# Performance work log

Measured on AMD Instinct MI355X. Metric: run time of the kernel, lower is better.

## Reference

```python
import jax, jax.numpy as jnp
import numpy as np

B, S, D = 2, 1024, 1024
H, HD = 16, 64
E_R = 31          # routed experts (n_experts - n_shared)
K_ACT = 3         # activated routed experts (n_activated - n_shared)
INTER = 1024      # expert inter dim = int(D*4*0.25)
EPS = 1e-5
BASE = 10000.0


def setup_inputs() -> dict:
    key = jax.random.key(0)
    ks = jax.random.split(key, 24)
    s = 0.02
    theta = (BASE ** (-jnp.arange(HD // 2, dtype=jnp.float32) * 2.0 / HD))
    inp = {
        'x': jax.random.normal(ks[0], (B, S, D), jnp.float32),
        'positions': jnp.arange(S, dtype=jnp.int32),
        'theta': theta,
        'gamma1': jnp.ones((D,), jnp.float32),
        'gamma2': jnp.ones((D,), jnp.float32),
        'q_w': jax.random.normal(ks[1], (D, H * HD), jnp.float32) * s,
        'q_b': jnp.zeros((H * HD,), jnp.float32),
        'k_w': jax.random.normal(ks[2], (D, H * HD), jnp.float32) * s,
        'k_b': jnp.zeros((H * HD,), jnp.float32),
        'v_w': jax.random.normal(ks[3], (D, H * HD), jnp.float32) * s,
        'v_b': jnp.zeros((H * HD,), jnp.float32),
        'o_w': jax.random.normal(ks[4], (H * HD, D), jnp.float32) * s,
        'o_b': jnp.zeros((D,), jnp.float32),
        'router_w': jax.random.normal(ks[5], (D, E_R), jnp.float32) * s,
        'router_b': jnp.zeros((E_R,), jnp.float32),
        'sh_w1': jax.random.normal(ks[6], (D, INTER), jnp.float32) * s,
        'sh_b1': jnp.zeros((INTER,), jnp.float32),
        'sh_w2': jax.random.normal(ks[7], (INTER, D), jnp.float32) * s,
        'sh_b2': jnp.zeros((D,), jnp.float32),
        're_w1': jax.random.normal(ks[8], (E_R, D, INTER), jnp.float32) * s,
        're_b1': jnp.zeros((E_R, INTER), jnp.float32),
        're_w2': jax.random.normal(ks[9], (E_R, INTER, D), jnp.float32) * s,
        're_b2': jnp.zeros((E_R, D), jnp.float32),
    }
    return inp


def _rmsnorm(x, gamma):
    rms = jnp.sqrt(jnp.mean(x * x, axis=-1, keepdims=True) + EPS)
    return x / rms * gamma


def _rope(x, theta):
    # x: [B,H,S,HD]; split even/odd, rotate, concat halves (matches source)
    seq = x.shape[2]
    angles = jnp.arange(seq, dtype=theta.dtype)[:, None] * theta  # [S, HD/2]
    cos = jnp.cos(angles)[None, None]
    sin = jnp.sin(angles)[None, None]
    x1, x2 = x[..., 0::2], x[..., 1::2]
    return jnp.concatenate([x1 * cos - x2 * sin, x1 * sin + x2 * cos], axis=-1)


def _forward(x, theta, gamma1, gamma2, q_w, q_b, k_w, k_b, v_w, v_b, o_w, o_b,
             router_w, router_b, sh_w1, sh_b1, sh_w2, sh_b2,
             re_w1, re_b1, re_w2, re_b2):
    b, s, d = x.shape
    xn = _rmsnorm(x, gamma1)
    # --- MHA ---
    q = (xn @ q_w + q_b).reshape(b, s, H, HD).transpose(0, 2, 1, 3)
    k = (xn @ k_w + k_b).reshape(b, s, H, HD).transpose(0, 2, 1, 3)
    v = (xn @ v_w + v_b).reshape(b, s, H, HD).transpose(0, 2, 1, 3)
    q = _rope(q, theta)
    k = _rope(k, theta)
    scale = 1.0 / np.sqrt(HD)
    scores = jnp.einsum('bhqd,bhkd->bhqk', q, k) * scale
    causal = jnp.tril(jnp.ones((s, s), dtype=bool))
    scores = jnp.where(causal, scores, -jnp.inf)
    attn = jax.nn.softmax(scores, axis=-1)
    ctx = jnp.einsum('bhqk,bhkd->bhqd', attn, v)
    ctx = ctx.transpose(0, 2, 1, 3).reshape(b, s, H * HD)
    attn_out = ctx @ o_w + o_b + xn
    # --- MoE ---
    an = _rmsnorm(attn_out, gamma2)
    shared = jax.nn.gelu(an @ sh_w1 + sh_b1, approximate=False) @ sh_w2 + sh_b2
    logits = an @ router_w + router_b                      # [B,S,E]
    aff = jax.nn.softmax(logits, axis=-1)
    topv, topi = jax.lax.top_k(aff, K_ACT)                 # [B,S,K]
    gates = jnp.sum(jax.nn.one_hot(topi, E_R, dtype=aff.dtype) * topv[..., None], axis=-2)  # [B,S,E]
    h = jax.nn.gelu(jnp.einsum('bsd,edh->besh', an, re_w1) + re_b1[None, :, None, :],
                    approximate=False)                     # [B,E,S,INTER]
    routed = jnp.einsum('bse,besh,ehd->bsd', gates, h, re_w2) \
           + jnp.einsum('bse,ed->bsd', gates, re_b2)
    return shared + routed + an + attn_out


def reference(x, positions, theta, gamma1, gamma2, q_w, q_b, k_w, k_b, v_w, v_b,
              o_w, o_b, router_w, router_b, sh_w1, sh_b1, sh_w2, sh_b2,
              re_w1, re_b1, re_w2, re_b2):
    del positions  # unused by the original forward (RoPE builds its own arange)
    return _forward(x, theta, gamma1, gamma2, q_w, q_b, k_w, k_b, v_w, v_b,
                    o_w, o_b, router_w, router_b, sh_w1, sh_b1, sh_w2, sh_b2,
                    re_w1, re_b1, re_w2, re_b2)
```

## Files before the change

### kernel.cpp

```cpp
#include <hip/hip_runtime.h>
#include <math.h>

typedef unsigned short u16;
typedef short s8v __attribute__((ext_vector_type(8)));
typedef u16 u4v __attribute__((ext_vector_type(4)));
typedef float f4v __attribute__((ext_vector_type(4)));

#define MFMA16(a,b,c) __builtin_amdgcn_mfma_f32_16x16x32_bf16((a),(b),(c),0,0,0)
#define GLDS16(g, l) __builtin_amdgcn_global_load_lds( \
    (const __attribute__((address_space(1))) unsigned int*)(g), \
    (__attribute__((address_space(3))) unsigned int*)(l), 16, 0, 0)

#define N_TOK 2048
#define SEQ   1024

__device__ __forceinline__ u16 f2b(float f){
  union { float f; unsigned u; } v; v.f = f;
  return (u16)((v.u + 0x7FFFu + ((v.u >> 16) & 1u)) >> 16);
}
__device__ __forceinline__ float b2f(u16 b){
  union { unsigned u; float f; } v; v.u = ((unsigned)b) << 16; return v.f;
}
__device__ __forceinline__ float gelu_f(float x){
  return 0.5f*x*(1.0f + erff(x*0.70710678118654752f));
}

__global__ __launch_bounds__(256) void rmsnorm_k(const float* __restrict__ x,
    const float* __restrict__ gamma, float* __restrict__ outf, u16* __restrict__ outb)
{
  const int t = blockIdx.x, tid = threadIdx.x;
  const float* xr = x + (size_t)t * 1024;
  float4 xv = *(const float4*)(xr + tid*4);
  float ss = xv.x*xv.x + xv.y*xv.y + xv.z*xv.z + xv.w*xv.w;
  #pragma unroll
  for (int off = 32; off; off >>= 1) ss += __shfl_down(ss, off);
  __shared__ float red[4];
  if ((tid & 63) == 0) red[tid >> 6] = ss;
  __syncthreads();
  float inv = rsqrtf((red[0]+red[1]+red[2]+red[3]) * (1.0f/1024.0f) + 1e-5f);
  float4 gv = *(const float4*)(gamma + tid*4);
  float4 o;
  o.x = xv.x*inv*gv.x; o.y = xv.y*inv*gv.y; o.z = xv.z*inv*gv.z; o.w = xv.w*inv*gv.w;
  *(float4*)(outf + (size_t)t*1024 + tid*4) = o;
  u4v ob = { f2b(o.x), f2b(o.y), f2b(o.z), f2b(o.w) };
  *(u4v*)(outb + (size_t)t*1024 + tid*4) = ob;
}

__global__ __launch_bounds__(256) void ropetab_k(const float* __restrict__ theta, float* __restrict__ tab)
{
  int i = blockIdx.x*256 + threadIdx.x;
  int s = i >> 5, j = i & 31;
  float sn, cs;
  sincosf((float)s * theta[j], &sn, &cs);
  tab[(size_t)s*64 + 2*j]     = cs;
  tab[(size_t)s*64 + 2*j + 1] = sn;
}

__device__ __forceinline__ void transT_body(const float* __restrict__ W, u16* __restrict__ Wt)
{
  __shared__ __align__(16) u16 T[64][68];
  const int tid = threadIdx.x;
  const int k0 = blockIdx.x*64, n0 = blockIdx.y*64;
  #pragma unroll
  for (int j = 0; j < 4; j++) {
    int q = j*256 + tid; int r = q >> 4, c4 = q & 15;
    float4 v = *(const float4*)(W + (size_t)(k0 + r)*1024 + n0 + c4*4);
    T[c4*4+0][r] = f2b(v.x); T[c4*4+1][r] = f2b(v.y);
    T[c4*4+2][r] = f2b(v.z); T[c4*4+3][r] = f2b(v.w);
  }
  __syncthreads();
  #pragma unroll
  for (int j = 0; j < 4; j++) {
    int q = j*256 + tid; int n = q >> 4, c4 = q & 15;
    u4v o = *(const u4v*)&T[n][c4*4];
    *(u4v*)(Wt + (size_t)(n0 + n)*1024 + k0 + c4*4) = o;
  }
}

__global__ __launch_bounds__(256) void transT6_k(
    const float* s0, const float* s1, const float* s2,
    const float* s3, const float* s4, const float* s5,
    u16* d0, u16* d1, u16* d2, u16* d3, u16* d4, u16* d5)
{
  const float* S; u16* D;
  switch (blockIdx.z) {
    case 0: S=s0; D=d0; break; case 1: S=s1; D=d1; break;
    case 2: S=s2; D=d2; break; case 3: S=s3; D=d3; break;
    case 4: S=s4; D=d4; break; default: S=s5; D=d5; break;
  }
  transT_body(S, D);
}

__global__ __launch_bounds__(256) void transv_k(const u16* __restrict__ vb, u16* __restrict__ vt)
{
  __shared__ __align__(16) u16 T[64][72];
  const int tid = threadIdx.x;
  const int s0 = blockIdx.x*64, bh = blockIdx.y, b = bh>>4, h = bh&15;
  #pragma unroll
  for (int j = 0; j < 16; j++) {
    int q = j*256 + tid; int r = q >> 6, c = q & 63;
    T[c][r] = vb[(size_t)(b*SEQ + s0 + r)*1024 + h*64 + c];
  }
  __syncthreads();
  #pragma unroll
  for (int i = 0; i < 2; i++) {
    int q = tid*2 + i; int rr = q >> 3, c8 = q & 7;
    *(s8v*)(vt + (size_t)(bh*64 + rr)*1024 + s0 + c8*8) = *(const s8v*)&T[rr][c8*8];
  }
}

template<int MODE, int BM, int BN>
__global__ __launch_bounds__(256) void mmk(
    const u16* __restrict__ A,
    const u16* __restrict__ Wt0, const u16* __restrict__ Wt1, const u16* __restrict__ Wt2,
    const float* __restrict__ bias0, const float* __restrict__ bias1, const float* __restrict__ bias2,
    float* __restrict__ outf, u16* __restrict__ outb0, u16* __restrict__ outb1, u16* __restrict__ outb2,
    const float* __restrict__ add1, const float* __restrict__ add2,
    const int* __restrict__ gidx, const float* __restrict__ gatel,
    const int* __restrict__ counts, const int* __restrict__ offs,
    const int* __restrict__ wl, const int* __restrict__ ntl,
    const float* __restrict__ theta, const float* __restrict__ wf)
{
  constexpr bool EW = (MODE == 5 || MODE == 6);
  constexpr int MF = BM/32, NF = BN/32;
  constexpr int CA = BM/32, CB = BN/32;
  constexpr int BST = EW ? 72 : 64;
  __shared__ __align__(16) u16 As[BM*64];
  __shared__ __align__(16) u16 Bs[BN*BST];
  __shared__ int toks[(MODE==5) ? BM : 1];
  __shared__ float gts[(MODE==6) ? BM : 1];

  const int tid = threadIdx.x;
  const int wave = tid >> 6, lane = tid & 63, quad = lane >> 4, l15 = lane & 15;
  int row0 = blockIdx.y * BM;
  int col0 = blockIdx.x * BN;
  const u16* Wt = Wt0;
  const float* bias = bias0;
  const u16* Ab = A;
  const float* Wf = wf;
  int wsel = 0, e = 0, cnt = 0, off_e = 0;

  if (MODE == 7) {
    wsel = blockIdx.x >> 3;
    col0 = (blockIdx.x & 7) * BN;
    Wt   = (wsel == 0) ? Wt0 : ((wsel == 1) ? Wt1 : Wt2);
    bias = (wsel == 0) ? bias0 : ((wsel == 1) ? bias1 : bias2);
  }
  if (EW) {
    if ((int)blockIdx.y >= ntl[0]) return;
    const int w = wl[blockIdx.y];
    e = w >> 8;
    row0 = (w & 255) * BM;
    cnt = counts[e];
    Wf = wf + (size_t)e * 1024 * 1024;
    bias = bias0 + e * 1024;
    off_e = offs[e];
    if (MODE == 6) Ab = A + (size_t)off_e * 1024;
    if (tid < BM) {
      int ok = (row0 + tid) < cnt;
      if (MODE == 5) toks[tid] = ok ? gidx[e * N_TOK + row0 + tid] : 0;
      if (MODE == 6) gts[tid]  = ok ? gatel[e * N_TOK + row0 + tid] : 0.f;
    }
    __syncthreads();
  }

  const int lr8 = lane >> 3;
  const int lk  = (lane & 7) * 8;
  const u16* aptr[CA];
  const u16* bptr[CB];
  #pragma unroll
  for (int c = 0; c < CA; c++) {
    const int ar = wave*(BM/4) + c*8 + lr8;
    long garow;
    if (MODE == 5) {
      garow = toks[ar];
    } else if (MODE == 6) {
      int rr = row0 + ar; if (rr >= cnt) rr = cnt - 1; garow = rr;
    } else {
      garow = row0 + ar;
    }
    aptr[c] = Ab + (size_t)garow * 1024 + lk;
  }
  if (!EW) {
    #pragma unroll
    for (int c = 0; c < CB; c++) {
      const int br = wave*(BN/4) + c*8 + lr8;
      bptr[c] = Wt + (size_t)(col0 + br) * 1024 + lk;
    }
  }

  const int ewnb = tid >> 3;
  const int ewkb = tid & 7;
  const float* ewp = EW ? (Wf + (size_t)(ewkb*8)*1024 + col0 + ewnb*4) : nullptr;

  f4v acc[MF][NF];
  #pragma unroll
  for (int i = 0; i < MF; i++)
    #pragma unroll
    for (int j = 0; j < NF; j++)
      acc[i][j] = (f4v){0.f,0.f,0.f,0.f};

  const int wr = (wave >> 1) * (BM/2), wc = (wave & 1) * (BN/2);

  for (int k0 = 0; k0 < 1024; k0 += 64) {
    float4 f[EW ? 8 : 1];
    if (EW) {
      const float* wp = ewp + (size_t)k0 * 1024;
      #pragma unroll
      for (int kk = 0; kk < 8; kk++)
        f[kk] = *(const float4*)(wp + (size_t)kk * 1024);
    }
    __syncthreads();
    #pragma unroll
    for (int c = 0; c < CA; c++) GLDS16(aptr[c] + k0, As + (wave*(BM/4) + c*8)*64);
    if (EW) {
      #pragma unroll
      for (int j = 0; j < 4; j++) {
        s8v h;
        #pragma unroll
        for (int kk = 0; kk < 8; kk++) {
          float fv = (j == 0) ? f[kk].x : (j == 1) ? f[kk].y : (j == 2) ? f[kk].z : f[kk].w;
          h[kk] = (short)f2b(fv);
        }
        *(s8v*)&Bs[(ewnb*4 + j)*BST + ewkb*8] = h;
      }
    } else {
      #pragma unroll
      for (int c = 0; c < CB; c++) GLDS16(bptr[c] + k0, Bs + (wave*(BN/4) + c*8)*64);
    }
    __syncthreads();
    s8v af[2][MF], bfr[2][NF];
    #pragma unroll
    for (int ks = 0; ks < 2; ks++) {
      #pragma unroll
      for (int mt = 0; mt < MF; mt++) af[ks][mt]  = *(const s8v*)&As[(wr + mt*16 + l15)*64 + ks*32 + quad*8];
      #pragma unroll
      for (int nt = 0; nt < NF; nt++) bfr[ks][nt] = *(const s8v*)&Bs[(wc + nt*16 + l15)*BST + ks*32 + quad*8];
    }
    #pragma unroll
    for (int ks = 0; ks < 2; ks++)
      #pragma unroll
      for (int mt = 0; mt < MF; mt++)
        #pragma unroll
        for (int nt = 0; nt < NF; nt++)
          acc[mt][nt] = MFMA16(af[ks][mt], bfr[ks][nt], acc[mt][nt]);
  }

  #pragma unroll
  for (int mt = 0; mt < MF; mt++) {
    #pragma unroll
    for (int reg = 0; reg < 4; reg++) {
      const int lr = wr + mt*16 + quad*4 + reg;
      const size_t gr = row0 + lr;
      #pragma unroll
      for (int nt = 0; nt < NF; nt++) {
        const int n = wc + nt*16 + l15 + col0;
        float v = acc[mt][nt][reg] + bias[n];
        if (MODE == 7) {
          if (wsel == 2) {
            outb2[gr*1024 + n] = f2b(v);
          } else {
            float pv = __shfl_xor(v, 1);
            const int hd = n & 63;
            const int j = hd >> 1;
            const int s = (int)(gr & (SEQ - 1));
            float2 t = *(const float2*)&theta[(size_t)s*64 + 2*j];
            float cs = t.x, sn = t.y;
            float res; int col;
            if (hd & 1) { res = pv*sn + v*cs; col = (n & ~63) | (32 + j); }
            else        { res = v*cs - pv*sn; col = (n & ~63) | j; }
            u16 bv = f2b(res);
            if (wsel == 0) outb0[gr*1024 + col] = bv;
            else           outb1[gr*1024 + col] = bv;
          }
        } else if (MODE == 3) {
          outf[gr*1024 + n] = v + add1[gr*1024 + n];
        } else if (MODE == 2) {
          outb0[gr*1024 + n] = f2b(gelu_f(v));
        } else if (MODE == 4) {
          outf[gr*1024 + n] = v + add1[gr*1024 + n] + add2[gr*1024 + n];
        } else if (MODE == 5) {
          if (row0 + lr < cnt)
            outb0[(size_t)(off_e + row0 + lr)*1024 + n] = f2b(gelu_f(v));
        } else if (MODE == 6) {
          if (row0 + lr < cnt)
            outf[(size_t)(off_e + row0 + lr)*1024 + n] = gts[lr] * v;
        }
      }
    }
  }
}

__global__ __launch_bounds__(256) void attn_k(const u16* __restrict__ qg,
    const u16* __restrict__ kg, const u16* __restrict__ vtg, u16* __restrict__ ctx)
{
  const int qt = (blockIdx.y < 16) ? blockIdx.x : (15 - blockIdx.x);
  const int bh = blockIdx.y, b = bh >> 4, h = bh & 15;
  const int tid = threadIdx.x, wave = tid >> 6, lane = tid & 63;
  const int quad = lane >> 4, l15 = lane & 15;
  __shared__ __align__(16) u16 Ks[64][72];
  __shared__ __align__(16) u16 Vt[64][72];
  __shared__ __align__(16) u16 Ps[4][16][72];

  s8v aq0, aq1;
  {
    const size_t qrow = (size_t)(b*SEQ + qt*64 + wave*16 + l15);
    aq0 = *(const s8v*)(qg + qrow*1024 + h*64 + quad*8);
    aq1 = *(const s8v*)(qg + qrow*1024 + h*64 + 32 + quad*8);
  }
  f4v oac[4];
  #pragma unroll
  for (int i = 0; i < 4; i++) oac[i] = (f4v){0.f,0.f,0.f,0.f};
  float mi[4] = {-INFINITY,-INFINITY,-INFINITY,-INFINITY};
  float li[4] = {0.f,0.f,0.f,0.f};

  for (int kt = 0; kt <= qt; kt++) {
    __syncthreads();
    #pragma unroll
    for (int ii = 0; ii < 2; ii++) {
      int c = tid*2 + ii, r = c >> 3, c8 = c & 7;
      *(s8v*)&Ks[r][c8*8] = *(const s8v*)(kg + (size_t)(b*SEQ + kt*64 + r)*1024 + h*64 + c8*8);
      *(s8v*)&Vt[r][c8*8] = *(const s8v*)(vtg + (size_t)(bh*64 + r)*1024 + kt*64 + c8*8);
    }
    __syncthreads();

    f4v s[4];
    #pragma unroll
    for (int nt = 0; nt < 4; nt++) {
      f4v z = (f4v){0.f,0.f,0.f,0.f};
      s8v bk0 = *(const s8v*)&Ks[nt*16 + l15][quad*8];
      s8v bk1 = *(const s8v*)&Ks[nt*16 + l15][32 + quad*8];
      z = MFMA16(aq0, bk0, z);
      z = MFMA16(aq1, bk1, z);
      s[nt] = z;
    }
    float sc[4][4];
    const int rowl = wave*16 + quad*4;
    #pragma unroll
    for (int nt = 0; nt < 4; nt++) {
      #pragma unroll
      for (int r = 0; r < 4; r++) {
        float v = s[nt][r] * 0.125f;
        if (kt == qt && (nt*16 + l15) > (rowl + r)) v = -INFINITY;
        sc[nt][r] = v;
      }
    }
    float alpha[4];
    #pragma unroll
    for (int r = 0; r < 4; r++) {
      float v0 = fmaxf(fmaxf(sc[0][r], sc[1][r]), fmaxf(sc[2][r], sc[3][r]));
      v0 = fmaxf(v0, __shfl_xor(v0, 1));
      v0 = fmaxf(v0, __shfl_xor(v0, 2));
      v0 = fmaxf(v0, __shfl_xor(v0, 4));
      v0 = fmaxf(v0, __shfl_xor(v0, 8));
      float mnew = fmaxf(mi[r], v0);
      alpha[r] = __expf(mi[r] - mnew);
      mi[r] = mnew;
    }
    float psum[4] = {0.f,0.f,0.f,0.f};
    #pragma unroll
    for (int nt = 0; nt < 4; nt++) {
      #pragma unroll
      for (int r = 0; r < 4; r++) {
        float p = __expf(sc[nt][r] - mi[r]);
        psum[r] += p;
        Ps[wave][quad*4 + r][nt*16 + l15] = f2b(p);
      }
    }
    #pragma unroll
    for (int r = 0; r < 4; r++) {
      float ps = psum[r];
      ps += __shfl_xor(ps, 1);
      ps += __shfl_xor(ps, 2);
      ps += __shfl_xor(ps, 4);
      ps += __shfl_xor(ps, 8);
      li[r] = li[r]*alpha[r] + ps;
    }
    #pragma unroll
    for (int ht = 0; ht < 4; ht++) {
      f4v o = oac[ht];
      o[0] *= alpha[0]; o[1] *= alpha[1]; o[2] *= alpha[2]; o[3] *= alpha[3];
      oac[ht] = o;
    }
    asm volatile("s_waitcnt lgkmcnt(0)" ::: "memory");
    s8v pf0 = *(const s8v*)&Ps[wave][l15][quad*8];
    s8v pf1 = *(const s8v*)&Ps[wave][l15][32 + quad*8];
    #pragma unroll
    for (int ht = 0; ht < 4; ht++) {
      s8v vf0 = *(const s8v*)&Vt[ht*16 + l15][quad*8];
      s8v vf1 = *(const s8v*)&Vt[ht*16 + l15][32 + quad*8];
      oac[ht] = MFMA16(pf0, vf0, oac[ht]);
      oac[ht] = MFMA16(pf1, vf1, oac[ht]);
    }
  }
  float inv[4];
  #pragma unroll
  for (int r = 0; r < 4; r++) inv[r] = 1.f / li[r];
  #pragma unroll
  for (int ht = 0; ht < 4; ht++) {
    #pragma unroll
    for (int r = 0; r < 4; r++) {
      size_t row = (size_t)(b*SEQ + qt*64 + wave*16 + quad*4 + r);
      ctx[row*1024 + h*64 + ht*16 + l15] = f2b(oac[ht][r] * inv[r]);
    }
  }
}

__global__ __launch_bounds__(256) void router_k(const float* __restrict__ an,
    const float* __restrict__ rw, const float* __restrict__ rb,
    int* __restrict__ counts, int* __restrict__ tok_list, float* __restrict__ gate_list,
    int* __restrict__ tok_e, int* __restrict__ tok_s)
{
  const int t = blockIdx.x, tid = threadIdx.x;
  const int e = tid & 31, ch = tid >> 5;
  float part = 0.f;
  if (e < 31) {
    const float* ar = an + (size_t)t*1024 + ch*128;
    const float* wp = rw + (size_t)(ch*128)*31 + e;
    #pragma unroll 8
    for (int d = 0; d < 128; d++) part += ar[d] * wp[d*31];
  }
  __shared__ float red[8][32];
  __shared__ float lgs[32];
  red[ch][e] = part;
  __syncthreads();
  if (tid < 31) {
    float s = 0.f;
    #pragma unroll
    for (int c = 0; c < 8; c++) s += red[c][tid];
    lgs[tid] = s + rb[tid];
  }
  __syncthreads();
  if (tid == 0) {
    float m = -1e30f;
    for (int i = 0; i < 31; i++) m = fmaxf(m, lgs[i]);
    float den = 0.f;
    for (int i = 0; i < 31; i++) den += __expf(lgs[i] - m);
    float invd = 1.f/den;
    unsigned used = 0;
    for (int kk = 0; kk < 3; kk++) {
      int best = 0; float bv = -3e30f;
      for (int i = 0; i < 31; i++) if (!((used>>i)&1u) && lgs[i] > bv) { bv = lgs[i]; best = i; }
      used |= (1u << best);
      float gate = __expf(lgs[best] - m) * invd;
      int slot = atomicAdd(&counts[best], 1);
      tok_list[best*N_TOK + slot] = t;
      gate_list[best*N_TOK + slot] = gate;
      tok_e[t*3 + kk] = best;
      tok_s[t*3 + kk] = slot;
    }
  }
}

__global__ void scan_k(const int* __restrict__ counts, int* __restrict__ offs,
                       int* __restrict__ wl, int* __restrict__ ntl){
  if (threadIdx.x == 0) {
    int s = 0, nt = 0;
    for (int i = 0; i < 31; i++){
      offs[i] = s; s += counts[i];
      int t = (counts[i] + 127) >> 7;
      for (int r = 0; r < t; r++) wl[nt++] = (i << 8) | r;
    }
    ntl[0] = nt;
  }
}

__global__ __launch_bounds__(256) void reduce_k(const float* __restrict__ mo,
    const int* __restrict__ tok_e, const int* __restrict__ tok_s,
    const int* __restrict__ offs, float* __restrict__ out)
{
  const int t = blockIdx.x, tid = threadIdx.x;
  float4 acc = *(const float4*)(out + (size_t)t*1024 + tid*4);
  #pragma unroll
  for (int j = 0; j < 3; j++) {
    int e = tok_e[t*3 + j], s = tok_s[t*3 + j];
    const float* row = mo + (size_t)(offs[e] + s) * 1024;
    float4 v = *(const float4*)(row + tid*4);
    acc.x += v.x; acc.y += v.y; acc.z += v.z; acc.w += v.w;
  }
  *(float4*)(out + (size_t)t*1024 + tid*4) = acc;
}

extern "C" void kernel_launch(void* const* d_in, const int* in_sizes, int n_in,
                              void* d_out, int out_size, void* d_ws, size_t ws_size,
                              hipStream_t stream)
{
  const float* x      = (const float*)d_in[0];
  const float* theta  = (const float*)d_in[2];
  const float* gamma1 = (const float*)d_in[3];
  const float* gamma2 = (const float*)d_in[4];
  const float* q_w = (const float*)d_in[5];
  const float* q_b = (const float*)d_in[6];
  const float* k_w = (const float*)d_in[7];
  const float* k_b = (const float*)d_in[8];
  const float* v_w = (const float*)d_in[9];
  const float* v_b = (const float*)d_in[10];
  const float* o_w = (const float*)d_in[11];
  const float* o_b = (const float*)d_in[12];
  const float* router_w = (const float*)d_in[13];
  const float* router_b = (const float*)d_in[14];
  const float* sh_w1 = (const float*)d_in[15];
  const float* sh_b1 = (const float*)d_in[16];
  const float* sh_w2 = (const float*)d_in[17];
  const float* sh_b2 = (const float*)d_in[18];
  const float* re_w1 = (const float*)d_in[19];
  const float* re_b1 = (const float*)d_in[20];
  const float* re_w2 = (const float*)d_in[21];
  const float* re_b2 = (const float*)d_in[22];
  float* out = (float*)d_out;

  char* p = (char*)d_ws;
  auto alloc = [&](size_t bytes) -> void* {
    void* r = (void*)p; p += (bytes + 255) & ~(size_t)255; return r;
  };
  const size_t F32 = (size_t)N_TOK*1024*4;
  const size_t B16 = (size_t)N_TOK*1024*2;
  float* xn       = (float*)alloc(F32);
  float* attn_out = (float*)alloc(F32);
  float* an       = (float*)alloc(F32);
  float* mo       = (float*)alloc((size_t)3*N_TOK*1024*4);
  u16* xnb  = (u16*)alloc(B16);
  u16* anb  = (u16*)alloc(B16);
  u16* vb   = (u16*)alloc(B16);
  u16* qb   = (u16*)alloc(B16);
  u16* kb   = (u16*)alloc(B16);
  u16* vt   = (u16*)alloc(B16);
  u16* ctxb = (u16*)alloc(B16);
  u16* shhb = (u16*)alloc(B16);
  u16* hmoe = (u16*)alloc((size_t)3*N_TOK*1024*2);
  u16* wtq  = (u16*)alloc((size_t)1024*1024*2);
  u16* wtk  = (u16*)alloc((size_t)1024*1024*2);
  u16* wtv  = (u16*)alloc((size_t)1024*1024*2);
  u16* wto  = (u16*)alloc((size_t)1024*1024*2);
  u16* wts1 = (u16*)alloc((size_t)1024*1024*2);
  u16* wts2 = (u16*)alloc((size_t)1024*1024*2);
  float* ropetab = (float*)alloc((size_t)SEQ*64*4);
  int* counts = (int*)alloc(128);
  int* offs   = (int*)alloc(128);
  int* tok_list  = (int*)alloc((size_t)31*N_TOK*4);
  float* gate_list = (float*)alloc((size_t)31*N_TOK*4);
  int* tok_e = (int*)alloc((size_t)N_TOK*3*4);
  int* tok_s = (int*)alloc((size_t)N_TOK*3*4);
  int* wl    = (int*)alloc(512);
  int* ntl   = (int*)alloc(64);

  hipMemsetAsync(counts, 0, 128, stream);

  transT6_k<<<dim3(16,16,6), 256, 0, stream>>>(q_w, k_w, v_w, o_w, sh_w1, sh_w2,
                                               wtq, wtk, wtv, wto, wts1, wts2);
  ropetab_k<<<(SEQ*32)/256, 256, 0, stream>>>(theta, ropetab);

  rmsnorm_k<<<N_TOK, 256, 0, stream>>>(x, gamma1, xn, xnb);

  mmk<7,64,128><<<dim3(24,32), 256, 0, stream>>>(xnb, wtq, wtk, wtv, q_b, k_b, v_b,
      nullptr, qb, kb, vb, nullptr, nullptr, nullptr, nullptr, nullptr, nullptr, nullptr, nullptr,
      ropetab, nullptr);

  transv_k<<<dim3(16,32), 256, 0, stream>>>(vb, vt);
  attn_k<<<dim3(16,32), 256, 0, stream>>>(qb, kb, vt, ctxb);

  mmk<3,64,64><<<dim3(16,32), 256, 0, stream>>>(ctxb, wto, nullptr, nullptr, o_b, nullptr, nullptr,
      attn_out, nullptr, nullptr, nullptr, xn, nullptr, nullptr, nullptr, nullptr, nullptr, nullptr, nullptr,
      nullptr, nullptr);

  rmsnorm_k<<<N_TOK, 256, 0, stream>>>(attn_out, gamma2, an, anb);

  mmk<2,64,64><<<dim3(16,32), 256, 0, stream>>>(anb, wts1, nullptr, nullptr, sh_b1, nullptr, nullptr,
      nullptr, shhb, nullptr, nullptr, nullptr, nullptr, nullptr, nullptr, nullptr, nullptr, nullptr, nullptr,
      nullptr, nullptr);

  router_k<<<N_TOK, 256, 0, stream>>>(an, router_w, router_b, counts, tok_list, gate_list, tok_e, tok_s);
  scan_k<<<1, 32, 0, stream>>>(counts, offs, wl, ntl);

  mmk<4,64,64><<<dim3(16,32), 256, 0, stream>>>(shhb, wts2, nullptr, nullptr, sh_b2, nullptr, nullptr,
      out, nullptr, nullptr, nullptr, an, attn_out, nullptr, nullptr, nullptr, nullptr, nullptr, nullptr,
      nullptr, nullptr);

  mmk<5,128,128><<<dim3(8,79), 256, 0, stream>>>(anb, nullptr, nullptr, nullptr, re_b1, nullptr, nullptr,
      nullptr, hmoe, nullptr, nullptr, nullptr, nullptr, tok_list, nullptr, counts, offs, wl, ntl,
      nullptr, re_w1);

  mmk<6,128,128><<<dim3(8,79), 256, 0, stream>>>(hmoe, nullptr, nullptr, nullptr, re_b2, nullptr, nullptr,
      mo, nullptr, nullptr, nullptr, nullptr, nullptr, tok_list, gate_list, counts, offs, wl, ntl,
      nullptr, re_w2);

  reduce_k<<<N_TOK, 256, 0, stream>>>(mo, tok_e, tok_s, offs, out);
}
```

Baseline: 564.4 us.

## Merge shared-expert and routed-expert GEMMs into combined launches with packed bf16 conversion

The shared-expert FFN GEMMs and the routed-expert grouped GEMMs now run in a single kernel launch per layer (fused_k), with blockIdx.y selecting dense or expert work. This cuts the launch count and lets the shared and routed work fill the GPU together. The shared GEMMs move from 64x64 to 128x128 tiles, and the fp32-to-bf16 weight conversion uses the packed v_cvt_pk_bf16_f32 instruction instead of scalar rounding. In exchange, the larger tiles give the dense part fewer blocks, and blocks with mixed work types may run unevenly.

```diff
diff --git a/kernel.cpp b/kernel.cpp
--- a/kernel.cpp
+++ b/kernel.cpp
@@ -5,6 +5,7 @@
 typedef short s8v __attribute__((ext_vector_type(8)));
 typedef u16 u4v __attribute__((ext_vector_type(4)));
 typedef float f4v __attribute__((ext_vector_type(4)));
+typedef unsigned u32x4 __attribute__((ext_vector_type(4)));
 
 #define MFMA16(a,b,c) __builtin_amdgcn_mfma_f32_16x16x32_bf16((a),(b),(c),0,0,0)
 #define GLDS16(g, l) __builtin_amdgcn_global_load_lds( \
@@ -115,20 +116,13 @@
     const u16* __restrict__ Wt0, const u16* __restrict__ Wt1, const u16* __restrict__ Wt2,
     const float* __restrict__ bias0, const float* __restrict__ bias1, const float* __restrict__ bias2,
     float* __restrict__ outf, u16* __restrict__ outb0, u16* __restrict__ outb1, u16* __restrict__ outb2,
-    const float* __restrict__ add1, const float* __restrict__ add2,
-    const int* __restrict__ gidx, const float* __restrict__ gatel,
-    const int* __restrict__ counts, const int* __restrict__ offs,
-    const int* __restrict__ wl, const int* __restrict__ ntl,
-    const float* __restrict__ theta, const float* __restrict__ wf)
-{
-  constexpr bool EW = (MODE == 5 || MODE == 6);
+    const float* __restrict__ add1,
+    const float* __restrict__ theta)
+{
   constexpr int MF = BM/32, NF = BN/32;
   constexpr int CA = BM/32, CB = BN/32;
-  constexpr int BST = EW ? 72 : 64;
   __shared__ __align__(16) u16 As[BM*64];
-  __shared__ __align__(16) u16 Bs[BN*BST];
-  __shared__ int toks[(MODE==5) ? BM : 1];
-  __shared__ float gts[(MODE==6) ? BM : 1];
+  __shared__ __align__(16) u16 Bs[BN*64];
 
   const int tid = threadIdx.x;
   const int wave = tid >> 6, lane = tid & 63, quad = lane >> 4, l15 = lane & 15;
@@ -136,9 +130,7 @@
   int col0 = blockIdx.x * BN;
   const u16* Wt = Wt0;
   const float* bias = bias0;
-  const u16* Ab = A;
-  const float* Wf = wf;
-  int wsel = 0, e = 0, cnt = 0, off_e = 0;
+  int wsel = 0;
 
   if (MODE == 7) {
     wsel = blockIdx.x >> 3;
@@ -146,23 +138,6 @@
     Wt   = (wsel == 0) ? Wt0 : ((wsel == 1) ? Wt1 : Wt2);
     bias = (wsel == 0) ? bias0 : ((wsel == 1) ? bias1 : bias2);
   }
-  if (EW) {
-    if ((int)blockIdx.y >= ntl[0]) return;
-    const int w = wl[blockIdx.y];
-    e = w >> 8;
-    row0 = (w & 255) * BM;
-    cnt = counts[e];
-    Wf = wf + (size_t)e * 1024 * 1024;
-    bias = bias0 + e * 1024;
-    off_e = offs[e];
-    if (MODE == 6) Ab = A + (size_t)off_e * 1024;
-    if (tid < BM) {
-      int ok = (row0 + tid) < cnt;
-      if (MODE == 5) toks[tid] = ok ? gidx[e * N_TOK + row0 + tid] : 0;
-      if (MODE == 6) gts[tid]  = ok ? gatel[e * N_TOK + row0 + tid] : 0.f;
-    }
-    __syncthreads();
-  }
 
   const int lr8 = lane >> 3;
   const int lk  = (lane & 7) * 8;
@@ -171,27 +146,13 @@
   #pragma unroll
   for (int c = 0; c < CA; c++) {
     const int ar = wave*(BM/4) + c*8 + lr8;
-    long garow;
-    if (MODE == 5) {
-      garow = toks[ar];
-    } else if (MODE == 6) {
-      int rr = row0 + ar; if (rr >= cnt) rr = cnt - 1; garow = rr;
-    } else {
-      garow = row0 + ar;
-    }
-    aptr[c] = Ab + (size_t)garow * 1024 + lk;
-  }
-  if (!EW) {
-    #pragma unroll
-    for (int c = 0; c < CB; c++) {
-      const int br = wave*(BN/4) + c*8 + lr8;
-      bptr[c] = Wt + (size_t)(col0 + br) * 1024 + lk;
-    }
-  }
-
-  const int ewnb = tid >> 3;
-  const int ewkb = tid & 7;
-  const float* ewp = EW ? (Wf + (size_t)(ewkb*8)*1024 + col0 + ewnb*4) : nullptr;
+    aptr[c] = A + (size_t)(row0 + ar) * 1024 + lk;
+  }
+  #pragma unroll
+  for (int c = 0; c < CB; c++) {
+    const int br = wave*(BN/4) + c*8 + lr8;
+    bptr[c] = Wt + (size_t)(col0 + br) * 1024 + lk;
+  }
 
   f4v acc[MF][NF];
   #pragma unroll
@@ -203,31 +164,11 @@
   const int wr = (wave >> 1) * (BM/2), wc = (wave & 1) * (BN/2);
 
   for (int k0 = 0; k0 < 1024; k0 += 64) {
-    float4 f[EW ? 8 : 1];
-    if (EW) {
-      const float* wp = ewp + (size_t)k0 * 1024;
-      #pragma unroll
-      for (int kk = 0; kk < 8; kk++)
-        f[kk] = *(const float4*)(wp + (size_t)kk * 1024);
-    }
     __syncthreads();
     #pragma unroll
     for (int c = 0; c < CA; c++) GLDS16(aptr[c] + k0, As + (wave*(BM/4) + c*8)*64);
-    if (EW) {
-      #pragma unroll
-      for (int j = 0; j < 4; j++) {
-        s8v h;
-        #pragma unroll
-        for (int kk = 0; kk < 8; kk++) {
-          float fv = (j == 0) ? f[kk].x : (j == 1) ? f[kk].y : (j == 2) ? f[kk].z : f[kk].w;
-          h[kk] = (short)f2b(fv);
-        }
-        *(s8v*)&Bs[(ewnb*4 + j)*BST + ewkb*8] = h;
-      }
-    } else {
-      #pragma unroll
-      for (int c = 0; c < CB; c++) GLDS16(bptr[c] + k0, Bs + (wave*(BN/4) + c*8)*64);
-    }
+    #pragma unroll
+    for (int c = 0; c < CB; c++) GLDS16(bptr[c] + k0, Bs + (wave*(BN/4) + c*8)*64);
     __syncthreads();
     s8v af[2][MF], bfr[2][NF];
     #pragma unroll
@@ -235,7 +176,7 @@
       #pragma unroll
       for (int mt = 0; mt < MF; mt++) af[ks][mt]  = *(const s8v*)&As[(wr + mt*16 + l15)*64 + ks*32 + quad*8];
       #pragma unroll
-      for (int nt = 0; nt < NF; nt++) bfr[ks][nt] = *(const s8v*)&Bs[(wc + nt*16 + l15)*BST + ks*32 + quad*8];
+      for (int nt = 0; nt < NF; nt++) bfr[ks][nt] = *(const s8v*)&Bs[(wc + nt*16 + l15)*64 + ks*32 + quad*8];
     }
     #pragma unroll
     for (int ks = 0; ks < 2; ks++)
@@ -275,16 +216,173 @@
           }
         } else if (MODE == 3) {
           outf[gr*1024 + n] = v + add1[gr*1024 + n];
-        } else if (MODE == 2) {
-          outb0[gr*1024 + n] = f2b(gelu_f(v));
-        } else if (MODE == 4) {
-          outf[gr*1024 + n] = v + add1[gr*1024 + n] + add2[gr*1024 + n];
-        } else if (MODE == 5) {
-          if (row0 + lr < cnt)
-            outb0[(size_t)(off_e + row0 + lr)*1024 + n] = f2b(gelu_f(v));
-        } else if (MODE == 6) {
-          if (row0 + lr < cnt)
-            outf[(size_t)(off_e + row0 + lr)*1024 + n] = gts[lr] * v;
+        }
+      }
+    }
+  }
+}
+
+template<int PAIR>
+__global__ __launch_bounds__(256) void fused_k(
+    const u16* __restrict__ Adn, const u16* __restrict__ Wt, const float* __restrict__ biasd,
+    u16* __restrict__ outbd, float* __restrict__ outfd,
+    const float* __restrict__ add1, const float* __restrict__ add2,
+    const u16* __restrict__ Amoe, const float* __restrict__ wf, const float* __restrict__ biase,
+    u16* __restrict__ outbe, float* __restrict__ outfe,
+    const int* __restrict__ gidx, const float* __restrict__ gatel,
+    const int* __restrict__ counts, const int* __restrict__ offs,
+    const int* __restrict__ wl, const int* __restrict__ ntl)
+{
+  __shared__ __align__(16) u16 As[128*64];
+  __shared__ __align__(16) u16 Bs[128*72];
+  __shared__ int toks[128];
+  __shared__ float gts[128];
+
+  const int tid = threadIdx.x;
+  const int wave = tid >> 6, lane = tid & 63, quad = lane >> 4, l15 = lane & 15;
+  const int wr = (wave >> 1) * 64, wc = (wave & 1) * 64;
+  const int col0 = blockIdx.x * 128;
+  const int lr8 = lane >> 3, lk = (lane & 7) * 8;
+
+  f4v acc[4][4];
+  #pragma unroll
+  for (int i = 0; i < 4; i++)
+    #pragma unroll
+    for (int j = 0; j < 4; j++)
+      acc[i][j] = (f4v){0.f,0.f,0.f,0.f};
+
+  if (blockIdx.y < 16) {
+    const int row0 = blockIdx.y * 128;
+    const u16 *ap[4], *bp[4];
+    #pragma unroll
+    for (int c = 0; c < 4; c++) {
+      const int ar = wave*32 + c*8 + lr8;
+      ap[c] = Adn + (size_t)(row0 + ar) * 1024 + lk;
+      bp[c] = Wt  + (size_t)(col0 + ar) * 1024 + lk;
+    }
+    for (int k0 = 0; k0 < 1024; k0 += 64) {
+      __syncthreads();
+      #pragma unroll
+      for (int c = 0; c < 4; c++) GLDS16(ap[c] + k0, As + (wave*32 + c*8)*64);
+      #pragma unroll
+      for (int c = 0; c < 4; c++) GLDS16(bp[c] + k0, Bs + (wave*32 + c*8)*64);
+      __syncthreads();
+      s8v af[2][4], bfr[2][4];
+      #pragma unroll
+      for (int ks = 0; ks < 2; ks++) {
+        #pragma unroll
+        for (int mt = 0; mt < 4; mt++) af[ks][mt]  = *(const s8v*)&As[(wr + mt*16 + l15)*64 + ks*32 + quad*8];
+        #pragma unroll
+        for (int nt = 0; nt < 4; nt++) bfr[ks][nt] = *(const s8v*)&Bs[(wc + nt*16 + l15)*64 + ks*32 + quad*8];
+      }
+      #pragma unroll
+      for (int ks = 0; ks < 2; ks++)
+        #pragma unroll
+        for (int mt = 0; mt < 4; mt++)
+          #pragma unroll
+          for (int nt = 0; nt < 4; nt++)
+            acc[mt][nt] = MFMA16(af[ks][mt], bfr[ks][nt], acc[mt][nt]);
+    }
+    #pragma unroll
+    for (int mt = 0; mt < 4; mt++) {
+      #pragma unroll
+      for (int reg = 0; reg < 4; reg++) {
+        const int lr = wr + mt*16 + quad*4 + reg;
+        const size_t gr = row0 + lr;
+        #pragma unroll
+        for (int nt = 0; nt < 4; nt++) {
+          const int n = wc + nt*16 + l15 + col0;
+          float v = acc[mt][nt][reg] + biasd[n];
+          if (PAIR == 0) outbd[gr*1024 + n] = f2b(gelu_f(v));
+          else           outfd[gr*1024 + n] = v + add1[gr*1024 + n] + add2[gr*1024 + n];
+        }
+      }
+    }
+  } else {
+    const int wy = blockIdx.y - 16;
+    if (wy >= ntl[0]) return;
+    const int w = wl[wy];
+    const int e = w >> 8;
+    const int row0 = (w & 255) * 128;
+    const int cnt = counts[e];
+    const float* Wf = wf + (size_t)e * 1024 * 1024;
+    const float* bias = biase + e * 1024;
+    const int off_e = offs[e];
+    const u16* Ab = (PAIR == 1) ? (Amoe + (size_t)off_e * 1024) : Amoe;
+    if (tid < 128) {
+      int ok = (row0 + tid) < cnt;
+      if (PAIR == 0) toks[tid] = ok ? gidx[e * N_TOK + row0 + tid] : 0;
+      else           gts[tid]  = ok ? gatel[e * N_TOK + row0 + tid] : 0.f;
+    }
+    __syncthreads();
+
+    const u16* ap[4];
+    #pragma unroll
+    for (int c = 0; c < 4; c++) {
+      const int ar = wave*32 + c*8 + lr8;
+      long garow;
+      if (PAIR == 0) garow = toks[ar];
+      else { int rr = row0 + ar; if (rr >= cnt) rr = cnt - 1; garow = rr; }
+      ap[c] = Ab + (size_t)garow * 1024 + lk;
+    }
+    const int ewnb = tid >> 3;
+    const int ewkb = tid & 7;
+    const float* ewp = Wf + (size_t)(ewkb*8)*1024 + col0 + ewnb*4;
+
+    for (int k0 = 0; k0 < 1024; k0 += 64) {
+      float4 f[8];
+      {
+        const float* wp = ewp + (size_t)k0 * 1024;
+        #pragma unroll
+        for (int kk = 0; kk < 8; kk++)
+          f[kk] = *(const float4*)(wp + (size_t)kk * 1024);
+      }
+      __syncthreads();
+      #pragma unroll
+      for (int c = 0; c < 4; c++) GLDS16(ap[c] + k0, As + (wave*32 + c*8)*64);
+      #pragma unroll
+      for (int j = 0; j < 4; j++) {
+        u32x4 wv;
+        #pragma unroll
+        for (int p = 0; p < 4; p++) {
+          float lo = ((const float*)&f[2*p])[j];
+          float hi = ((const float*)&f[2*p+1])[j];
+          unsigned r;
+          asm("v_cvt_pk_bf16_f32 %0, %1, %2" : "=v"(r) : "v"(lo), "v"(hi));
+          wv[p] = r;
+        }
+        *(u32x4*)&Bs[(ewnb*4 + j)*72 + ewkb*8] = wv;
+      }
+      __syncthreads();
+      s8v af[2][4], bfr[2][4];
+      #pragma unroll
+      for (int ks = 0; ks < 2; ks++) {
+        #pragma unroll
+        for (int mt = 0; mt < 4; mt++) af[ks][mt]  = *(const s8v*)&As[(wr + mt*16 + l15)*64 + ks*32 + quad*8];
+        #pragma unroll
+        for (int nt = 0; nt < 4; nt++) bfr[ks][nt] = *(const s8v*)&Bs[(wc + nt*16 + l15)*72 + ks*32 + quad*8];
+      }
+      #pragma unroll
+      for (int ks = 0; ks < 2; ks++)
+        #pragma unroll
+        for (int mt = 0; mt < 4; mt++)
+          #pragma unroll
+          for (int nt = 0; nt < 4; nt++)
+            acc[mt][nt] = MFMA16(af[ks][mt], bfr[ks][nt], acc[mt][nt]);
+    }
+    #pragma unroll
+    for (int mt = 0; mt < 4; mt++) {
+      #pragma unroll
+      for (int reg = 0; reg < 4; reg++) {
+        const int lr = wr + mt*16 + quad*4 + reg;
+        if (row0 + lr < cnt) {
+          #pragma unroll
+          for (int nt = 0; nt < 4; nt++) {
+            const int n = wc + nt*16 + l15 + col0;
+            float v = acc[mt][nt][reg] + bias[n];
+            if (PAIR == 0) outbe[(size_t)(off_e + row0 + lr)*1024 + n] = f2b(gelu_f(v));
+            else           outfe[(size_t)(off_e + row0 + lr)*1024 + n] = gts[lr] * v;
+          }
         }
       }
     }
@@ -553,36 +651,28 @@
   rmsnorm_k<<<N_TOK, 256, 0, stream>>>(x, gamma1, xn, xnb);
 
   mmk<7,64,128><<<dim3(24,32), 256, 0, stream>>>(xnb, wtq, wtk, wtv, q_b, k_b, v_b,
-      nullptr, qb, kb, vb, nullptr, nullptr, nullptr, nullptr, nullptr, nullptr, nullptr, nullptr,
-      ropetab, nullptr);
+      nullptr, qb, kb, vb, nullptr, ropetab);
 
   transv_k<<<dim3(16,32), 256, 0, stream>>>(vb, vt);
   attn_k<<<dim3(16,32), 256, 0, stream>>>(qb, kb, vt, ctxb);
 
   mmk<3,64,64><<<dim3(16,32), 256, 0, stream>>>(ctxb, wto, nullptr, nullptr, o_b, nullptr, nullptr,
-      attn_out, nullptr, nullptr, nullptr, xn, nullptr, nullptr, nullptr, nullptr, nullptr, nullptr, nullptr,
-      nullptr, nullptr);
+      attn_out, nullptr, nullptr, nullptr, xn, nullptr);
 
   rmsnorm_k<<<N_TOK, 256, 0, stream>>>(attn_out, gamma2, an, anb);
-
-  mmk<2,64,64><<<dim3(16,32), 256, 0, stream>>>(anb, wts1, nullptr, nullptr, sh_b1, nullptr, nullptr,
-      nullptr, shhb, nullptr, nullptr, nullptr, nullptr, nullptr, nullptr, nullptr, nullptr, nullptr, nullptr,
-      nullptr, nullptr);
 
   router_k<<<N_TOK, 256, 0, stream>>>(an, router_w, router_b, counts, tok_list, gate_list, tok_e, tok_s);
   scan_k<<<1, 32, 0, stream>>>(counts, offs, wl, ntl);
 
-  mmk<4,64,64><<<dim3(16,32), 256, 0, stream>>>(shhb, wts2, nullptr, nullptr, sh_b2, nullptr, nullptr,
-      out, nullptr, nullptr, nullptr, an, attn_out, nullptr, nullptr, nullptr, nullptr, nullptr, nullptr,
-      nullptr, nullptr);
-
-  mmk<5,128,128><<<dim3(8,79), 256, 0, stream>>>(anb, nullptr, nullptr, nullptr, re_b1, nullptr, nullptr,
-      nullptr, hmoe, nullptr, nullptr, nullptr, nullptr, tok_list, nullptr, counts, offs, wl, ntl,
-      nullptr, re_w1);
-
-  mmk<6,128,128><<<dim3(8,79), 256, 0, stream>>>(hmoe, nullptr, nullptr, nullptr, re_b2, nullptr, nullptr,
-      mo, nullptr, nullptr, nullptr, nullptr, nullptr, tok_list, gate_list, counts, offs, wl, ntl,
-      nullptr, re_w2);
+  fused_k<0><<<dim3(8, 16+79), 256, 0, stream>>>(
+      anb, wts1, sh_b1, shhb, nullptr, nullptr, nullptr,
+      anb, re_w1, re_b1, hmoe, nullptr,
+      tok_list, nullptr, counts, offs, wl, ntl);
+
+  fused_k<1><<<dim3(8, 16+79), 256, 0, stream>>>(
+      shhb, wts2, sh_b2, nullptr, out, an, attn_out,
+      hmoe, re_w2, re_b2, nullptr, mo,
+      nullptr, gate_list, counts, offs, wl, ntl);
 
   reduce_k<<<N_TOK, 256, 0, stream>>>(mo, tok_e, tok_s, offs, out);
 }
```

Result: slower. 587.8 us (+4.1%).
